# Optimization experiments

Hardware: AMD Instinct MI355X
Metric: run time of the kernel (lower is better)

The kernel has to match this reference:

```python
import jax, jax.numpy as jnp
import numpy as np

B, H, S, D = 4, 16, 2048, 64


def setup_inputs() -> dict:
    key = jax.random.key(0)
    kq, kk, kv = jax.random.split(key, 3)
    Q = jax.random.normal(kq, (B, H, S, D), dtype=jnp.float32)
    K = jax.random.normal(kk, (B, H, S, D), dtype=jnp.float32)
    V = jax.random.normal(kv, (B, H, S, D), dtype=jnp.float32)
    # causal mask, broadcasts over (B, H); True = keep, False (==0) = mask out
    mask = jnp.tril(jnp.ones((S, S), dtype=bool))
    return {"Q": Q, "K": K, "V": V, "mask": mask}


def reference(Q, K, V, mask):
    d_k = Q.shape[-1]
    scale = 1.0 / jnp.sqrt(jnp.asarray(d_k, dtype=Q.dtype))
    # [B,H,Sq,Sk] score matrix (the module materializes this fully)
    scores = jnp.einsum('bhqd,bhkd->bhqk', Q, K) * scale
    if mask is not None:
        scores = jnp.where(mask, scores, -jnp.inf)
    attn = jax.nn.softmax(scores, axis=-1)
    return jnp.einsum('bhqk,bhkd->bhqd', attn, V)
```

## Files before the change

kernel.cpp:

```cpp
#include <hip/hip_runtime.h>
#include <math.h>

namespace {

constexpr int SEQ   = 2048;
constexpr int DH    = 64;
constexpr int KVBLK = 64;
constexpr int BH    = 64;
constexpr int PADB  = 72;

typedef __bf16 bf16x8 __attribute__((ext_vector_type(8)));
typedef float  f32x16 __attribute__((ext_vector_type(16)));

union FragB { bf16x8 v; unsigned u[4]; };

__device__ __forceinline__ unsigned pack2(float a, float b) {
  unsigned r;
  asm("v_cvt_pk_bf16_f32 %0, %1, %2" : "=v"(r) : "v"(a), "v"(b));
  return r;
}

__device__ __forceinline__ void swap32(int a, int b, int &x, int &y) {
#if __has_builtin(__builtin_amdgcn_permlane32_swap)
  auto r = __builtin_amdgcn_permlane32_swap(a, b, false, false);
  x = r[0]; y = r[1];
#else
  const bool hi = ((threadIdx.x & 63) >= 32);
  const int sa = __shfl_xor(a, 32), sb = __shfl_xor(b, 32);
  x = hi ? sb : a;
  y = hi ? b  : sa;
#endif
}

__device__ __forceinline__ float xhalf_sum(float v) {
  int x, y; swap32(__float_as_int(v), __float_as_int(v), x, y);
  return __int_as_float(x) + __int_as_float(y);
}

__global__ __launch_bounds__(256, 2)
void attn_fwd(const float* __restrict__ Qg, const float* __restrict__ Kg,
              const float* __restrict__ Vg, float* __restrict__ Og)
{
  const int b   = blockIdx.x;
  const int bh  = b & 63;
  const int qi  = 31 - (b >> 6);
  const int NT  = qi + 1;

  const int tid  = threadIdx.x;
  const int wv   = tid >> 6;
  const int rw   = wv & 1;
  const int kh   = wv >> 1;
  const int lane = tid & 63;
  const int l31  = lane & 31;
  const int hi   = lane >> 5;
  const int qloc = rw * 32 + l31;

  const size_t base = (size_t)bh * SEQ * DH;
  const float* Qp = Qg + base;
  const float* Kp = Kg + base;
  const float* Vp = Vg + base;
  float*       Op = Og + base;

  __shared__ __align__(16) unsigned char smem[18432];
  auto K_lds  = reinterpret_cast<__bf16(*)[PADB]>(smem);
  auto Vt_lds = reinterpret_cast<__bf16(*)[PADB]>(smem + 9216);

  const float qscale = 0.125f * 1.44269504088896f;
  FragB bq[4];
  {
    const float* src = Qp + (size_t)(qi*64 + rw*32 + l31) * DH + hi*8;
#pragma unroll
    for (int ks = 0; ks < 4; ++ks) {
      float4 f0 = *(const float4*)(src + ks*16);
      float4 f1 = *(const float4*)(src + ks*16 + 4);
      bq[ks].u[0] = pack2(f0.x*qscale, f0.y*qscale);
      bq[ks].u[1] = pack2(f0.z*qscale, f0.w*qscale);
      bq[ks].u[2] = pack2(f1.x*qscale, f1.y*qscale);
      bq[ks].u[3] = pack2(f1.z*qscale, f1.w*qscale);
    }
  }

  float4 kr[2][2];
  float  vr[16];
  const int kc8 = tid & 7;
  const int vd  = tid & 63;
  const int vk0 = (tid >> 6) * 16;

  auto load_tile = [&](int tile) {
    const int kvb = tile * KVBLK;
#pragma unroll
    for (int p = 0; p < 2; ++p) {
      const float* s = Kp + (size_t)(kvb + 32*p + (tid >> 3)) * DH + kc8*8;
      kr[p][0] = *(const float4*)s;
      kr[p][1] = *(const float4*)(s + 4);
    }
#pragma unroll
    for (int r = 0; r < 16; ++r)
      vr[r] = Vp[(size_t)(kvb + vk0 + r) * DH + vd];
  };

  auto store_tile = [&]() {
#pragma unroll
    for (int p = 0; p < 2; ++p) {
      uint4 w;
      w.x = pack2(kr[p][0].x, kr[p][0].y); w.y = pack2(kr[p][0].z, kr[p][0].w);
      w.z = pack2(kr[p][1].x, kr[p][1].y); w.w = pack2(kr[p][1].z, kr[p][1].w);
      *reinterpret_cast<uint4*>(&K_lds[32*p + (tid >> 3)][kc8*8]) = w;
    }
    uint4 w0, w1;
    w0.x = pack2(vr[0],  vr[1]);  w0.y = pack2(vr[2],  vr[3]);
    w0.z = pack2(vr[4],  vr[5]);  w0.w = pack2(vr[6],  vr[7]);
    w1.x = pack2(vr[8],  vr[9]);  w1.y = pack2(vr[10], vr[11]);
    w1.z = pack2(vr[12], vr[13]); w1.w = pack2(vr[14], vr[15]);
    *reinterpret_cast<uint4*>(&Vt_lds[vd][vk0])     = w0;
    *reinterpret_cast<uint4*>(&Vt_lds[vd][vk0 + 8]) = w1;
  };

  f32x16 oacc[2];
#pragma unroll
  for (int dt = 0; dt < 2; ++dt)
#pragma unroll
    for (int r = 0; r < 16; ++r) oacc[dt][r] = 0.f;
  float lpart = 0.f;

  load_tile(0);
  store_tile();
  __syncthreads();

  for (int t = 0; t < NT; ++t) {
    if (t + 1 < NT) load_tile(t + 1);
    const bool diag = (t == NT - 1);

    f32x16 st;
#pragma unroll
    for (int r = 0; r < 16; ++r) st[r] = 0.f;
    __builtin_amdgcn_s_setprio(1);
#pragma unroll
    for (int ks = 0; ks < 4; ++ks) {
      bf16x8 ak = *(const bf16x8*)&K_lds[kh*32 + l31][ks*16 + hi*8];
      st = __builtin_amdgcn_mfma_f32_32x32x16_bf16(ak, bq[ks].v, st, 0, 0, 0);
    }
    __builtin_amdgcn_s_setprio(0);

    float p[16];
#pragma unroll
    for (int r = 0; r < 16; ++r) {
      float s = st[r];
      if (diag) {
        const int kvl = kh*32 + (r & 3) + 4*hi + 8*(r >> 2);
        if (kvl > qloc) s = -INFINITY;
      }
      const float e = exp2f(s);
      p[r] = e;
      lpart += e;
    }

    unsigned pk[8];
#pragma unroll
    for (int j2 = 0; j2 < 8; ++j2) pk[j2] = pack2(p[2*j2], p[2*j2 + 1]);

    FragB pa[2];
#pragma unroll
    for (int ks2 = 0; ks2 < 2; ++ks2) {
      const int gA = 2*ks2, gB = 2*ks2 + 1;
      int x0, y0, x1, y1;
      swap32((int)pk[2*gA],     (int)pk[2*gB],     x0, y0);
      swap32((int)pk[2*gA + 1], (int)pk[2*gB + 1], x1, y1);
      pa[ks2].u[0] = (unsigned)x0;
      pa[ks2].u[1] = (unsigned)x1;
      pa[ks2].u[2] = (unsigned)y0;
      pa[ks2].u[3] = (unsigned)y1;
    }

    __builtin_amdgcn_s_setprio(1);
#pragma unroll
    for (int dt = 0; dt < 2; ++dt)
#pragma unroll
      for (int ks2 = 0; ks2 < 2; ++ks2) {
        bf16x8 av = *(const bf16x8*)&Vt_lds[dt*32 + l31][kh*32 + ks2*16 + hi*8];
        oacc[dt] = __builtin_amdgcn_mfma_f32_32x32x16_bf16(av, pa[ks2].v, oacc[dt], 0, 0, 0);
      }
    __builtin_amdgcn_s_setprio(0);

    __syncthreads();
    if (t + 1 < NT) {
      store_tile();
      __syncthreads();
    }
  }

  {
    float* reg0 = reinterpret_cast<float*>(smem);
    float* reg1 = reinterpret_cast<float*>(smem + 9216);
    float* myreg = rw ? reg1 : reg0;
    const int rb = l31 * 68;

    if (kh == 1) {
#pragma unroll
      for (int dt = 0; dt < 2; ++dt)
#pragma unroll
        for (int g4 = 0; g4 < 4; ++g4) {
          float4 w;
          w.x = oacc[dt][4*g4 + 0]; w.y = oacc[dt][4*g4 + 1];
          w.z = oacc[dt][4*g4 + 2]; w.w = oacc[dt][4*g4 + 3];
          *(float4*)&myreg[rb + dt*32 + 8*g4 + 4*hi] = w;
        }
      const float s1 = xhalf_sum(lpart);
      if (hi == 0) myreg[rb + 64] = s1;
    }
    __syncthreads();
    if (kh == 0) {
      const float linv = 1.0f / (xhalf_sum(lpart) + myreg[rb + 64]);
#pragma unroll
      for (int dt = 0; dt < 2; ++dt)
#pragma unroll
        for (int g4 = 0; g4 < 4; ++g4) {
          float4 v = *(const float4*)&myreg[rb + dt*32 + 8*g4 + 4*hi];
          v.x = (v.x + oacc[dt][4*g4 + 0]) * linv;
          v.y = (v.y + oacc[dt][4*g4 + 1]) * linv;
          v.z = (v.z + oacc[dt][4*g4 + 2]) * linv;
          v.w = (v.w + oacc[dt][4*g4 + 3]) * linv;
          *(float4*)&myreg[rb + dt*32 + 8*g4 + 4*hi] = v;
        }
    }
    __syncthreads();
    {
      float* dst = Op + (size_t)(qi * 64) * DH;
#pragma unroll
      for (int i = 0; i < 4; ++i) {
        const int f   = tid + i*256;
        const int row = f >> 4;
        const int ch  = f & 15;
        const float* srcrow = (row < 32) ? (reg0 + row*68) : (reg1 + (row-32)*68);
        float4 v = *(const float4*)&srcrow[ch*4];
        *(float4*)&dst[(size_t)row*DH + ch*4] = v;
      }
    }
  }
}

}

extern "C" void kernel_launch(void* const* d_in, const int* in_sizes, int n_in,
                              void* d_out, int out_size, void* d_ws, size_t ws_size,
                              hipStream_t stream) {
  const float* Q = (const float*)d_in[0];
  const float* K = (const float*)d_in[1];
  const float* V = (const float*)d_in[2];
  float* O = (float*)d_out;
  attn_fwd<<<dim3(32 * BH), dim3(256), 0, stream>>>(Q, K, V, O);
}
```

Baseline: 88.35 us.

## Pre-convert K/V to swizzled bf16 workspace and stream tiles via direct global-to-LDS loads

Adds a prep kernel that converts K to bf16 with an XOR-swizzled layout and V to a transposed, swizzled bf16 layout in the workspace. The attention kernel then double-buffers 64-row tiles straight into LDS with global_load_lds, removing per-tile register staging, conversion and transposed V scatter from the main loop. It also halves the bytes the attention kernel reads for K/V. The cost is an extra launch plus a full read/write of K and V, 32KB LDS per block, and a fallback kernel when the workspace is too small.

```diff
diff --git a/kernel.cpp b/kernel.cpp
--- a/kernel.cpp
+++ b/kernel.cpp
@@ -7,7 +7,7 @@
 constexpr int DH    = 64;
 constexpr int KVBLK = 64;
 constexpr int BH    = 64;
-constexpr int PADB  = 72;
+constexpr size_t WS_NEED = (size_t)BH * SEQ * DH * 2  * 2 ;
 
 typedef __bf16 bf16x8 __attribute__((ext_vector_type(8)));
 typedef float  f32x16 __attribute__((ext_vector_type(16)));
@@ -18,6 +18,12 @@
   unsigned r;
   asm("v_cvt_pk_bf16_f32 %0, %1, %2" : "=v"(r) : "v"(a), "v"(b));
   return r;
+}
+
+__device__ __forceinline__ unsigned short bf16c(float f) {
+  union { float f; unsigned u; } v; v.f = f;
+  unsigned r = v.u + 0x7fffu + ((v.u >> 16) & 1u);
+  return (unsigned short)(r >> 16);
 }
 
 __device__ __forceinline__ void swap32(int a, int b, int &x, int &y) {
@@ -37,9 +43,61 @@
   return __int_as_float(x) + __int_as_float(y);
 }
 
+__device__ __forceinline__ void gload16(const void* g, void* l) {
+  __builtin_amdgcn_global_load_lds(
+      (const __attribute__((address_space(1))) void*)g,
+      (__attribute__((address_space(3))) void*)l, 16, 0, 0);
+}
+
+__global__ __launch_bounds__(256)
+void prep(const float* __restrict__ Kg, const float* __restrict__ Vg,
+          unsigned short* __restrict__ wsK, unsigned short* __restrict__ wsV)
+{
+  const int blk = blockIdx.x;
+  const int bh  = blk & 63;
+  const int t   = blk >> 6;
+  const int tid = threadIdx.x;
+
+  const float* Kb = Kg + (size_t)bh * SEQ * DH;
+  unsigned short* wK = wsK + (size_t)bh * SEQ * DH;
+#pragma unroll
+  for (int i = 0; i < 2; ++i) {
+    const int kc  = tid + i * 256;
+    const int row = kc >> 3, c = kc & 7;
+    const int csrc = c ^ (row & 7);
+    const float* s = Kb + (size_t)(t*64 + row) * DH + csrc * 8;
+    float4 a = *(const float4*)s, b2 = *(const float4*)(s + 4);
+    uint4 w;
+    w.x = pack2(a.x, a.y);   w.y = pack2(a.z, a.w);
+    w.z = pack2(b2.x, b2.y); w.w = pack2(b2.z, b2.w);
+    *(uint4*)&wK[(size_t)(t*64 + row) * DH + c * 8] = w;
+  }
+
+  __shared__ unsigned short vt[64 * 64];
+  const float* Vb = Vg + (size_t)bh * SEQ * DH;
+  {
+    const int kv = tid >> 2;
+    const int d0 = (tid & 3) * 16;
+    const float* s = Vb + (size_t)(t*64 + kv) * DH + d0;
+#pragma unroll
+    for (int e = 0; e < 16; ++e) {
+      const int d = d0 + e;
+      const int slot = (kv >> 3) ^ (d & 7);
+      vt[d*64 + slot*8 + (kv & 7)] = bf16c(s[e]);
+    }
+  }
+  __syncthreads();
+  unsigned short* wV = wsV + (size_t)bh * SEQ * DH + (size_t)t * 4096;
+#pragma unroll
+  for (int i = 0; i < 2; ++i) {
+    const int o = (tid + i * 256) * 8;
+    *(uint4*)&wV[o] = *(const uint4*)&vt[o];
+  }
+}
+
 __global__ __launch_bounds__(256, 2)
-void attn_fwd(const float* __restrict__ Qg, const float* __restrict__ Kg,
-              const float* __restrict__ Vg, float* __restrict__ Og)
+void attn_fwd(const float* __restrict__ Qg, const unsigned short* __restrict__ wsK,
+              const unsigned short* __restrict__ wsV, float* __restrict__ Og)
 {
   const int b   = blockIdx.x;
   const int bh  = b & 63;
@@ -55,15 +113,12 @@
   const int hi   = lane >> 5;
   const int qloc = rw * 32 + l31;
 
-  const size_t base = (size_t)bh * SEQ * DH;
-  const float* Qp = Qg + base;
-  const float* Kp = Kg + base;
-  const float* Vp = Vg + base;
-  float*       Op = Og + base;
-
-  __shared__ __align__(16) unsigned char smem[18432];
-  auto K_lds  = reinterpret_cast<__bf16(*)[PADB]>(smem);
-  auto Vt_lds = reinterpret_cast<__bf16(*)[PADB]>(smem + 9216);
+  const float* Qp = Qg + (size_t)bh * SEQ * DH;
+  const unsigned short* Kw = wsK + (size_t)bh * SEQ * DH;
+  const unsigned short* Vw = wsV + (size_t)bh * SEQ * DH;
+  float* Op = Og + (size_t)bh * SEQ * DH;
+
+  __shared__ __align__(16) unsigned char smem[32768];
 
   const float qscale = 0.125f * 1.44269504088896f;
   FragB bq[4];
@@ -80,42 +135,6 @@
     }
   }
 
-  float4 kr[2][2];
-  float  vr[16];
-  const int kc8 = tid & 7;
-  const int vd  = tid & 63;
-  const int vk0 = (tid >> 6) * 16;
-
-  auto load_tile = [&](int tile) {
-    const int kvb = tile * KVBLK;
-#pragma unroll
-    for (int p = 0; p < 2; ++p) {
-      const float* s = Kp + (size_t)(kvb + 32*p + (tid >> 3)) * DH + kc8*8;
-      kr[p][0] = *(const float4*)s;
-      kr[p][1] = *(const float4*)(s + 4);
-    }
-#pragma unroll
-    for (int r = 0; r < 16; ++r)
-      vr[r] = Vp[(size_t)(kvb + vk0 + r) * DH + vd];
-  };
-
-  auto store_tile = [&]() {
-#pragma unroll
-    for (int p = 0; p < 2; ++p) {
-      uint4 w;
-      w.x = pack2(kr[p][0].x, kr[p][0].y); w.y = pack2(kr[p][0].z, kr[p][0].w);
-      w.z = pack2(kr[p][1].x, kr[p][1].y); w.w = pack2(kr[p][1].z, kr[p][1].w);
-      *reinterpret_cast<uint4*>(&K_lds[32*p + (tid >> 3)][kc8*8]) = w;
-    }
-    uint4 w0, w1;
-    w0.x = pack2(vr[0],  vr[1]);  w0.y = pack2(vr[2],  vr[3]);
-    w0.z = pack2(vr[4],  vr[5]);  w0.w = pack2(vr[6],  vr[7]);
-    w1.x = pack2(vr[8],  vr[9]);  w1.y = pack2(vr[10], vr[11]);
-    w1.z = pack2(vr[12], vr[13]); w1.w = pack2(vr[14], vr[15]);
-    *reinterpret_cast<uint4*>(&Vt_lds[vd][vk0])     = w0;
-    *reinterpret_cast<uint4*>(&Vt_lds[vd][vk0 + 8]) = w1;
-  };
-
   f32x16 oacc[2];
 #pragma unroll
   for (int dt = 0; dt < 2; ++dt)
@@ -123,13 +142,20 @@
     for (int r = 0; r < 16; ++r) oacc[dt][r] = 0.f;
   float lpart = 0.f;
 
-  load_tile(0);
-  store_tile();
-  __syncthreads();
-
-  for (int t = 0; t < NT; ++t) {
-    if (t + 1 < NT) load_tile(t + 1);
-    const bool diag = (t == NT - 1);
+  auto stage = [&](int tile, int bufoff) {
+    const unsigned short* gK = Kw + (size_t)tile * 4096 + wv*512 + lane*8;
+    const unsigned short* gV = Vw + (size_t)tile * 4096 + wv*512 + lane*8;
+    char* lb = (char*)smem + bufoff + wv*1024;
+    gload16(gK,        lb);
+    gload16(gK + 2048, lb + 4096);
+    gload16(gV,        lb + 8192);
+    gload16(gV + 2048, lb + 12288);
+  };
+
+  auto compute = [&](bool diag, int bufoff) {
+    const unsigned short* Kl = (const unsigned short*)(smem + bufoff);
+    const unsigned short* Vl = (const unsigned short*)(smem + bufoff + 8192);
+    const int krow = kh*32 + l31;
 
     f32x16 st;
 #pragma unroll
@@ -137,7 +163,7 @@
     __builtin_amdgcn_s_setprio(1);
 #pragma unroll
     for (int ks = 0; ks < 4; ++ks) {
-      bf16x8 ak = *(const bf16x8*)&K_lds[kh*32 + l31][ks*16 + hi*8];
+      bf16x8 ak = *(const bf16x8*)&Kl[krow*64 + (((2*ks + hi) ^ (krow & 7)) * 8)];
       st = __builtin_amdgcn_mfma_f32_32x32x16_bf16(ak, bq[ks].v, st, 0, 0, 0);
     }
     __builtin_amdgcn_s_setprio(0);
@@ -174,24 +200,34 @@
 
     __builtin_amdgcn_s_setprio(1);
 #pragma unroll
-    for (int dt = 0; dt < 2; ++dt)
+    for (int dt = 0; dt < 2; ++dt) {
+      const int d = dt*32 + l31;
 #pragma unroll
       for (int ks2 = 0; ks2 < 2; ++ks2) {
-        bf16x8 av = *(const bf16x8*)&Vt_lds[dt*32 + l31][kh*32 + ks2*16 + hi*8];
+        bf16x8 av = *(const bf16x8*)&Vl[d*64 + (((4*kh + 2*ks2 + hi) ^ (d & 7)) * 8)];
         oacc[dt] = __builtin_amdgcn_mfma_f32_32x32x16_bf16(av, pa[ks2].v, oacc[dt], 0, 0, 0);
       }
+    }
     __builtin_amdgcn_s_setprio(0);
-
+  };
+
+  stage(0, 0);
+  __syncthreads();
+
+  for (int t = 0; t < NT; t += 2) {
+    if (t + 1 < NT) stage(t + 1, 16384);
+    compute(t == NT - 1, 0);
     __syncthreads();
     if (t + 1 < NT) {
-      store_tile();
+      if (t + 2 < NT) stage(t + 2, 0);
+      compute(t + 1 == NT - 1, 16384);
       __syncthreads();
     }
   }
 
   {
     float* reg0 = reinterpret_cast<float*>(smem);
-    float* reg1 = reinterpret_cast<float*>(smem + 9216);
+    float* reg1 = reinterpret_cast<float*>(smem + 16384);
     float* myreg = rw ? reg1 : reg0;
     const int rb = l31 * 68;
 
@@ -239,6 +275,205 @@
   }
 }
 
+constexpr int PADB = 72;
+
+__global__ __launch_bounds__(256, 2)
+void attn_fb(const float* __restrict__ Qg, const float* __restrict__ Kg,
+             const float* __restrict__ Vg, float* __restrict__ Og)
+{
+  const int b   = blockIdx.x;
+  const int bh  = b & 63;
+  const int qi  = 31 - (b >> 6);
+  const int NT  = qi + 1;
+  const int tid  = threadIdx.x;
+  const int wv   = tid >> 6;
+  const int rw   = wv & 1;
+  const int kh   = wv >> 1;
+  const int lane = tid & 63;
+  const int l31  = lane & 31;
+  const int hi   = lane >> 5;
+  const int qloc = rw * 32 + l31;
+
+  const size_t base = (size_t)bh * SEQ * DH;
+  const float* Qp = Qg + base;
+  const float* Kp = Kg + base;
+  const float* Vp = Vg + base;
+  float*       Op = Og + base;
+
+  __shared__ __align__(16) unsigned char smem[18432];
+  auto K_lds  = reinterpret_cast<__bf16(*)[PADB]>(smem);
+  auto Vt_lds = reinterpret_cast<__bf16(*)[PADB]>(smem + 9216);
+
+  const float qscale = 0.125f * 1.44269504088896f;
+  FragB bq[4];
+  {
+    const float* src = Qp + (size_t)(qi*64 + rw*32 + l31) * DH + hi*8;
+#pragma unroll
+    for (int ks = 0; ks < 4; ++ks) {
+      float4 f0 = *(const float4*)(src + ks*16);
+      float4 f1 = *(const float4*)(src + ks*16 + 4);
+      bq[ks].u[0] = pack2(f0.x*qscale, f0.y*qscale);
+      bq[ks].u[1] = pack2(f0.z*qscale, f0.w*qscale);
+      bq[ks].u[2] = pack2(f1.x*qscale, f1.y*qscale);
+      bq[ks].u[3] = pack2(f1.z*qscale, f1.w*qscale);
+    }
+  }
+
+  float4 kr[2][2];
+  float  vr[16];
+  const int kc8 = tid & 7;
+  const int vd  = tid & 63;
+  const int vk0 = (tid >> 6) * 16;
+
+  auto load_tile = [&](int tile) {
+    const int kvb = tile * KVBLK;
+#pragma unroll
+    for (int p = 0; p < 2; ++p) {
+      const float* s = Kp + (size_t)(kvb + 32*p + (tid >> 3)) * DH + kc8*8;
+      kr[p][0] = *(const float4*)s;
+      kr[p][1] = *(const float4*)(s + 4);
+    }
+#pragma unroll
+    for (int r = 0; r < 16; ++r)
+      vr[r] = Vp[(size_t)(kvb + vk0 + r) * DH + vd];
+  };
+
+  auto store_tile = [&]() {
+#pragma unroll
+    for (int p = 0; p < 2; ++p) {
+      uint4 w;
+      w.x = pack2(kr[p][0].x, kr[p][0].y); w.y = pack2(kr[p][0].z, kr[p][0].w);
+      w.z = pack2(kr[p][1].x, kr[p][1].y); w.w = pack2(kr[p][1].z, kr[p][1].w);
+      *reinterpret_cast<uint4*>(&K_lds[32*p + (tid >> 3)][kc8*8]) = w;
+    }
+    uint4 w0, w1;
+    w0.x = pack2(vr[0],  vr[1]);  w0.y = pack2(vr[2],  vr[3]);
+    w0.z = pack2(vr[4],  vr[5]);  w0.w = pack2(vr[6],  vr[7]);
+    w1.x = pack2(vr[8],  vr[9]);  w1.y = pack2(vr[10], vr[11]);
+    w1.z = pack2(vr[12], vr[13]); w1.w = pack2(vr[14], vr[15]);
+    *reinterpret_cast<uint4*>(&Vt_lds[vd][vk0])     = w0;
+    *reinterpret_cast<uint4*>(&Vt_lds[vd][vk0 + 8]) = w1;
+  };
+
+  f32x16 oacc[2];
+#pragma unroll
+  for (int dt = 0; dt < 2; ++dt)
+#pragma unroll
+    for (int r = 0; r < 16; ++r) oacc[dt][r] = 0.f;
+  float lpart = 0.f;
+
+  load_tile(0);
+  store_tile();
+  __syncthreads();
+
+  for (int t = 0; t < NT; ++t) {
+    if (t + 1 < NT) load_tile(t + 1);
+    const bool diag = (t == NT - 1);
+
+    f32x16 st;
+#pragma unroll
+    for (int r = 0; r < 16; ++r) st[r] = 0.f;
+#pragma unroll
+    for (int ks = 0; ks < 4; ++ks) {
+      bf16x8 ak = *(const bf16x8*)&K_lds[kh*32 + l31][ks*16 + hi*8];
+      st = __builtin_amdgcn_mfma_f32_32x32x16_bf16(ak, bq[ks].v, st, 0, 0, 0);
+    }
+
+    float p[16];
+#pragma unroll
+    for (int r = 0; r < 16; ++r) {
+      float s = st[r];
+      if (diag) {
+        const int kvl = kh*32 + (r & 3) + 4*hi + 8*(r >> 2);
+        if (kvl > qloc) s = -INFINITY;
+      }
+      const float e = exp2f(s);
+      p[r] = e;
+      lpart += e;
+    }
+
+    unsigned pk[8];
+#pragma unroll
+    for (int j2 = 0; j2 < 8; ++j2) pk[j2] = pack2(p[2*j2], p[2*j2 + 1]);
+
+    FragB pa[2];
+#pragma unroll
+    for (int ks2 = 0; ks2 < 2; ++ks2) {
+      const int gA = 2*ks2, gB = 2*ks2 + 1;
+      int x0, y0, x1, y1;
+      swap32((int)pk[2*gA],     (int)pk[2*gB],     x0, y0);
+      swap32((int)pk[2*gA + 1], (int)pk[2*gB + 1], x1, y1);
+      pa[ks2].u[0] = (unsigned)x0;
+      pa[ks2].u[1] = (unsigned)x1;
+      pa[ks2].u[2] = (unsigned)y0;
+      pa[ks2].u[3] = (unsigned)y1;
+    }
+
+#pragma unroll
+    for (int dt = 0; dt < 2; ++dt)
+#pragma unroll
+      for (int ks2 = 0; ks2 < 2; ++ks2) {
+        bf16x8 av = *(const bf16x8*)&Vt_lds[dt*32 + l31][kh*32 + ks2*16 + hi*8];
+        oacc[dt] = __builtin_amdgcn_mfma_f32_32x32x16_bf16(av, pa[ks2].v, oacc[dt], 0, 0, 0);
+      }
+
+    __syncthreads();
+    if (t + 1 < NT) {
+      store_tile();
+      __syncthreads();
+    }
+  }
+
+  {
+    float* reg0 = reinterpret_cast<float*>(smem);
+    float* reg1 = reinterpret_cast<float*>(smem + 9216);
+    float* myreg = rw ? reg1 : reg0;
+    const int rb = l31 * 68;
+
+    if (kh == 1) {
+#pragma unroll
+      for (int dt = 0; dt < 2; ++dt)
+#pragma unroll
+        for (int g4 = 0; g4 < 4; ++g4) {
+          float4 w;
+          w.x = oacc[dt][4*g4 + 0]; w.y = oacc[dt][4*g4 + 1];
+          w.z = oacc[dt][4*g4 + 2]; w.w = oacc[dt][4*g4 + 3];
+          *(float4*)&myreg[rb + dt*32 + 8*g4 + 4*hi] = w;
+        }
+      const float s1 = xhalf_sum(lpart);
+      if (hi == 0) myreg[rb + 64] = s1;
+    }
+    __syncthreads();
+    if (kh == 0) {
+      const float linv = 1.0f / (xhalf_sum(lpart) + myreg[rb + 64]);
+#pragma unroll
+      for (int dt = 0; dt < 2; ++dt)
+#pragma unroll
+        for (int g4 = 0; g4 < 4; ++g4) {
+          float4 v = *(const float4*)&myreg[rb + dt*32 + 8*g4 + 4*hi];
+          v.x = (v.x + oacc[dt][4*g4 + 0]) * linv;
+          v.y = (v.y + oacc[dt][4*g4 + 1]) * linv;
+          v.z = (v.z + oacc[dt][4*g4 + 2]) * linv;
+          v.w = (v.w + oacc[dt][4*g4 + 3]) * linv;
+          *(float4*)&myreg[rb + dt*32 + 8*g4 + 4*hi] = v;
+        }
+    }
+    __syncthreads();
+    {
+      float* dst = Op + (size_t)(qi * 64) * DH;
+#pragma unroll
+      for (int i = 0; i < 4; ++i) {
+        const int f   = tid + i*256;
+        const int row = f >> 4;
+        const int ch  = f & 15;
+        const float* srcrow = (row < 32) ? (reg0 + row*68) : (reg1 + (row-32)*68);
+        float4 v = *(const float4*)&srcrow[ch*4];
+        *(float4*)&dst[(size_t)row*DH + ch*4] = v;
+      }
+    }
+  }
+}
+
 }
 
 extern "C" void kernel_launch(void* const* d_in, const int* in_sizes, int n_in,
@@ -248,5 +483,12 @@
   const float* K = (const float*)d_in[1];
   const float* V = (const float*)d_in[2];
   float* O = (float*)d_out;
-  attn_fwd<<<dim3(32 * BH), dim3(256), 0, stream>>>(Q, K, V, O);
-}
+  if (ws_size >= WS_NEED) {
+    unsigned short* wsK = (unsigned short*)d_ws;
+    unsigned short* wsV = wsK + (size_t)BH * SEQ * DH;
+    prep<<<dim3(BH * 32), dim3(256), 0, stream>>>(K, V, wsK, wsV);
+    attn_fwd<<<dim3(32 * BH), dim3(256), 0, stream>>>(Q, wsK, wsV, O);
+  } else {
+    attn_fb<<<dim3(32 * BH), dim3(256), 0, stream>>>(Q, K, V, O);
+  }
+}
```

Result: faster. 81.23 us (median of 2 runs) (-8.1%).
